# Optimization experiments

Hardware: AMD Instinct MI355X
Metric: run time of the kernel (lower is better)

Reference implementation:

```python
import jax, jax.numpy as jnp
import numpy as np

WS = (2, 7, 7)   # window size (d, h, w)
NH = 4           # num heads
EPS = 1e-5       # LayerNorm eps (torch default)


def _rel_index():
    wd, wh, ww = WS
    coords = np.stack(np.meshgrid(np.arange(wd), np.arange(wh), np.arange(ww), indexing='ij'))  # (3,wd,wh,ww)
    cf = coords.reshape(3, -1)                      # (3, N)
    rel = cf[:, :, None] - cf[:, None, :]           # (3, N, N)
    rel = rel.transpose(1, 2, 0).astype(np.int64)   # (N, N, 3)
    rel[..., 0] += wd - 1
    rel[..., 1] += wh - 1
    rel[..., 2] += ww - 1
    rel[..., 0] *= (2 * wh - 1) * (2 * ww - 1)
    rel[..., 1] *= (2 * ww - 1)
    return jnp.asarray(rel.sum(-1), dtype=jnp.int32)  # (N, N)


def setup_inputs() -> dict:
    key = jax.random.key(0)
    ks = jax.random.split(key, 6)
    C, CH = 128, 512
    TBL = (2 * WS[0] - 1) * (2 * WS[1] - 1) * (2 * WS[2] - 1)  # 507
    rn = lambda k, s, sc=0.02: jax.random.normal(k, s, jnp.float32) * sc
    return {
        'x': jax.random.normal(ks[0], (2, 8, 56, 56, C), jnp.float32),
        'norm1_w': jnp.ones((C,), jnp.float32), 'norm1_b': jnp.zeros((C,), jnp.float32),
        'qkv_w': rn(ks[1], (3 * C, C)), 'qkv_b': jnp.zeros((3 * C,), jnp.float32),
        'bias_table': rn(ks[2], (TBL, NH)),
        'proj_w': rn(ks[3], (C, C)), 'proj_b': jnp.zeros((C,), jnp.float32),
        'norm2_w': jnp.ones((C,), jnp.float32), 'norm2_b': jnp.zeros((C,), jnp.float32),
        'fc1_w': rn(ks[4], (CH, C)), 'fc1_b': jnp.zeros((CH,), jnp.float32),
        'fc2_w': rn(ks[5], (C, CH)), 'fc2_b': jnp.zeros((C,), jnp.float32),
        'rel_index': _rel_index(),
    }


def _layernorm(x, w, b):
    m = jnp.mean(x, axis=-1, keepdims=True)
    v = jnp.mean(jnp.square(x - m), axis=-1, keepdims=True)
    return (x - m) * jax.lax.rsqrt(v + EPS) * w + b


def reference(x, norm1_w, norm1_b, qkv_w, qkv_b, bias_table, proj_w, proj_b,
              norm2_w, norm2_b, fc1_w, fc1_b, fc2_w, fc2_b, rel_index):
    B, D, H, W, C = x.shape
    wd, wh, ww = WS
    N = wd * wh * ww
    hd = C // NH

    shortcut = x
    xn = _layernorm(x, norm1_w, norm1_b)
    # window partition: (B,D,H,W,C) -> (B*nW, N, C)
    xw = xn.reshape(B, D // wd, wd, H // wh, wh, W // ww, ww, C)
    xw = xw.transpose(0, 1, 3, 5, 2, 4, 6, 7).reshape(-1, N, C)
    B_ = xw.shape[0]

    qkv = (xw @ qkv_w.T + qkv_b).reshape(B_, N, 3, NH, hd).transpose(2, 0, 3, 1, 4)
    q, k, v = qkv[0] * (hd ** -0.5), qkv[1], qkv[2]   # (B_, NH, N, hd)
    attn = jnp.einsum('bhnd,bhmd->bhnm', q, k)
    bias = bias_table[rel_index.reshape(-1)].reshape(N, N, NH).transpose(2, 0, 1)  # (NH,N,N)
    attn = jax.nn.softmax(attn + bias[None], axis=-1)
    out = jnp.einsum('bhnm,bhmd->bhnd', attn, v).transpose(0, 2, 1, 3).reshape(B_, N, C)
    out = out @ proj_w.T + proj_b

    # window reverse: (B*nW, N, C) -> (B,D,H,W,C)
    xr = out.reshape(B, D // wd, H // wh, W // ww, wd, wh, ww, C)
    xr = xr.transpose(0, 1, 4, 2, 5, 3, 6, 7).reshape(B, D, H, W, C)

    x = shortcut + xr
    h = _layernorm(x, norm2_w, norm2_b)
    h = jax.nn.gelu(h @ fc1_w.T + fc1_b, approximate=False)  # torch nn.GELU = exact erf
    return x + (h @ fc2_w.T + fc2_b)
```

## Files before the change

### kernel.cpp

```cpp
#include <hip/hip_runtime.h>
#include <hip/hip_bf16.h>

typedef __hip_bfloat16 bf16;
typedef unsigned short u16t;
typedef unsigned int u32t;
typedef __attribute__((ext_vector_type(8))) short bf16x8_t;
typedef __attribute__((ext_vector_type(4))) float f32x4_t;

#define DEVI static __device__ __forceinline__

DEVI float u2f(u32t bits) { union { u32t u; float f; } v; v.u = bits; return v.f; }
DEVI float bflo(u32t u) { return u2f((u & 0xffffu) << 16); }
DEVI float bfhi(u32t u) { return u2f(u & 0xffff0000u); }
DEVI float sh2f(short s) { return u2f(((u32t)(u16t)s) << 16); }
DEVI float bf2f(bf16 h) { return __bfloat162float(h); }
DEVI bf16 f2bf(float f) { return __float2bfloat16(f); }
DEVI u16t f2bfbits(float f) {
  bf16 h = __float2bfloat16(f);
  union { bf16 h; u16t u; } v; v.h = h; return v.u;
}

DEVI void gl_lds16(const void* g, void* l) {
  __builtin_amdgcn_global_load_lds(
      (const __attribute__((address_space(1))) unsigned int*)g,
      (__attribute__((address_space(3))) unsigned int*)l, 16, 0, 0);
}

#define TOK   50176
#define NWIN  512
#define NTOK  98
#define NHEAD 4
#define HDIM  32
#define QSCALE 0.17677669529663687f

__global__ __launch_bounds__(256) void cvt4_k(
    const float* __restrict__ a, const float* __restrict__ b,
    const float* __restrict__ c, const float* __restrict__ d,
    bf16* __restrict__ o) {
  int i = blockIdx.x * 256 + threadIdx.x;
  const float* s; int off;
  if (i < 49152)       { s = a; off = 0; }
  else if (i < 65536)  { s = b; off = 49152; }
  else if (i < 131072) { s = c; off = 65536; }
  else                 { s = d; off = 131072; }
  float v = s[i - off];
  if (i < 16384) v *= QSCALE;
  o[i] = f2bf(v);
}

__global__ __launch_bounds__(256) void bias_k(const float* __restrict__ btab,
                                              const int* __restrict__ relidx,
                                              const float* __restrict__ qkv_b,
                                              float* __restrict__ BmatT,
                                              float* __restrict__ bsc) {
  int idx = blockIdx.x * 256 + threadIdx.x;
  if (idx < NTOK * NTOK) {
    int i = idx / NTOK, j = idx - i * NTOK;
    int r = relidx[idx] * NHEAD;
#pragma unroll
    for (int h = 0; h < NHEAD; h++)
      BmatT[(size_t)(h * NTOK + j) * 112 + i] = btab[r + h];
  }
  if (blockIdx.x == 0 && threadIdx.x < 384)
    bsc[threadIdx.x] = qkv_b[threadIdx.x] * (threadIdx.x < 128 ? QSCALE : 1.0f);
}

__global__ __launch_bounds__(256) void ln1_k(
    const float* __restrict__ x, const float* __restrict__ w,
    const float* __restrict__ b, bf16* __restrict__ o)
{
  const int wave = threadIdx.x >> 6, lane = threadIdx.x & 63;
  const int t = blockIdx.x * 4 + wave;
  const int c = lane << 1;
  float2 xv = *(const float2*)(x + (size_t)t * 128 + c);
  float x0 = xv.x, x1 = xv.y;
  float s = x0 + x1, ss = x0 * x0 + x1 * x1;
#pragma unroll
  for (int m = 32; m; m >>= 1) { s += __shfl_xor(s, m); ss += __shfl_xor(ss, m); }
  float mean = s * 0.0078125f;
  float var = ss * 0.0078125f - mean * mean;
  float rstd = rsqrtf(var + 1e-5f);
  float y0 = (x0 - mean) * rstd * w[c]     + b[c];
  float y1 = (x1 - mean) * rstd * w[c + 1] + b[c + 1];
  int wi = t % 56; int r = t / 56;
  int hi_ = r % 56; r /= 56;
  int di = r & 7; int bi = r >> 3;
  int nw = ((bi * 4 + (di >> 1)) * 8 + hi_ / 7) * 8 + wi / 7;
  int n  = ((di & 1) * 7 + hi_ % 7) * 7 + wi % 7;
  u32t ov = ((u32t)f2bfbits(y1) << 16) | (u32t)f2bfbits(y0);
  *(u32t*)((u16t*)o + (size_t)(nw * NTOK + n) * 128 + c) = ov;
}

DEVI int winrev(int grow) {
  int nw = grow / NTOK, n = grow - nw * NTOK;
  int wq = nw & 7, hq = (nw >> 3) & 7, dq = (nw >> 6) & 3, bb = nw >> 8;
  int wr = n % 7; int q7 = n / 7; int hr = q7 % 7, dr = q7 / 7;
  return ((bb * 8 + dq * 2 + dr) * 56 + hq * 7 + hr) * 56 + wq * 7 + wr;
}

template <int MODE, int NT16, int KT>
__global__ __launch_bounds__(256) void gemm3_k(
    const bf16* __restrict__ A, const bf16* __restrict__ W,
    const float* __restrict__ bias, const float* __restrict__ resX,
    const bf16* __restrict__ resB2, bf16* __restrict__ outB,
    bf16* __restrict__ outB2, float* __restrict__ outF,
    const float* __restrict__ lnw, const float* __restrict__ lnb, int N)
{
  __shared__ __align__(16) short As[128 * 128];
  __shared__ __align__(16) short Bs[NT16 * 16 * 128];
  const int K = KT * 128;
  const int tid = threadIdx.x;
  const int rowBase = blockIdx.y << 7;
  const int colBase = blockIdx.x * (NT16 * 16);
  const int wv = tid >> 6, lane = tid & 63;
  const int q = lane >> 4, r16 = lane & 15;
  const int mB = wv << 5;

  f32x4_t acc[2][NT16];
#pragma unroll
  for (int i = 0; i < 2; i++)
#pragma unroll
    for (int j = 0; j < NT16; j++) acc[i][j] = (f32x4_t){0.f, 0.f, 0.f, 0.f};

#pragma unroll
  for (int kt = 0; kt < KT; kt++) {
    const int kc = kt << 7;
#pragma unroll
    for (int t = 0; t < 8; t++) {
      int f = tid + (t << 8);
      int row = f >> 4, cs = (f & 15) ^ (row & 15);
      gl_lds16((const u16t*)A + (size_t)(rowBase + row) * K + kc + (cs << 3),
               &As[f << 3]);
    }
#pragma unroll
    for (int t = 0; t < NT16; t++) {
      int f = tid + (t << 8);
      int row = f >> 4, cs = (f & 15) ^ (row & 15);
      gl_lds16((const u16t*)W + (size_t)(colBase + row) * K + kc + (cs << 3),
               &Bs[f << 3]);
    }
    __syncthreads();
#pragma unroll
    for (int ks = 0; ks < 4; ks++) {
      bf16x8_t af[2], bfr[NT16];
#pragma unroll
      for (int mt = 0; mt < 2; mt++) {
        int row = mB + (mt << 4) + r16;
        int slot = ((ks << 2) + q) ^ (row & 15);
        af[mt] = *(const bf16x8_t*)&As[(row << 7) + (slot << 3)];
      }
#pragma unroll
      for (int nt = 0; nt < NT16; nt++) {
        int row = (nt << 4) + r16;
        int slot = ((ks << 2) + q) ^ (row & 15);
        bfr[nt] = *(const bf16x8_t*)&Bs[(row << 7) + (slot << 3)];
      }
#pragma unroll
      for (int mt = 0; mt < 2; mt++)
#pragma unroll
        for (int nt = 0; nt < NT16; nt++)
          acc[mt][nt] = __builtin_amdgcn_mfma_f32_16x16x32_bf16(
              af[mt], bfr[nt], acc[mt][nt], 0, 0, 0);
    }
    __syncthreads();
  }

  float bv[NT16];
#pragma unroll
  for (int nt = 0; nt < NT16; nt++) bv[nt] = bias[colBase + (nt << 4) + r16];

  if (MODE == 3) {
    float* Cf = (float*)As;
#pragma unroll
    for (int mt = 0; mt < 2; mt++)
#pragma unroll
      for (int reg = 0; reg < 4; reg++) {
        int lrow = mB + (mt << 4) + (q << 2) + reg;
#pragma unroll
        for (int nt = 0; nt < NT16; nt++)
          Cf[(lrow << 6) + (nt << 4) + r16] = acc[mt][nt][reg] + bv[nt];
      }
    __syncthreads();
#pragma unroll
    for (int t = 0; t < 8; t++) {
      int f = tid + (t << 8);
      int row = f >> 4, c4 = (f & 15) << 2;
      size_t ob = (size_t)(rowBase + row) * N + colBase + c4;
      const u16t* rp = (const u16t*)resB2 + ob;
      float4 v;
      v.x = Cf[(row << 6) + c4]     + sh2f(rp[0]);
      v.y = Cf[(row << 6) + c4 + 1] + sh2f(rp[1]);
      v.z = Cf[(row << 6) + c4 + 2] + sh2f(rp[2]);
      v.w = Cf[(row << 6) + c4 + 3] + sh2f(rp[3]);
      *(float4*)(outF + ob) = v;
    }
    return;
  }

  if (MODE == 1) {
#pragma unroll
    for (int mt = 0; mt < 2; mt++)
#pragma unroll
      for (int reg = 0; reg < 4; reg++) {
        int lrow = mB + (mt << 4) + (q << 2) + reg;
#pragma unroll
        for (int nt = 0; nt < NT16; nt++)
          As[(lrow << 7) + (nt << 4) + r16] = (short)f2bfbits(acc[mt][nt][reg] + bv[nt]);
      }
    __syncthreads();
#pragma unroll
    for (int t = 0; t < 8; t++) {
      int f = tid + (t << 8);
      int row = f >> 4, c8 = (f & 15) << 3;
      int tt = winrev(rowBase + row);
      size_t ob = (size_t)tt * 128 + c8;
      float4 r0 = *(const float4*)(resX + ob);
      float4 r1 = *(const float4*)(resX + ob + 4);
      short* cs = &As[(row << 7) + c8];
      u16t pk[8];
      pk[0] = f2bfbits(sh2f(cs[0]) + r0.x); pk[1] = f2bfbits(sh2f(cs[1]) + r0.y);
      pk[2] = f2bfbits(sh2f(cs[2]) + r0.z); pk[3] = f2bfbits(sh2f(cs[3]) + r0.w);
      pk[4] = f2bfbits(sh2f(cs[4]) + r1.x); pk[5] = f2bfbits(sh2f(cs[5]) + r1.y);
      pk[6] = f2bfbits(sh2f(cs[6]) + r1.z); pk[7] = f2bfbits(sh2f(cs[7]) + r1.w);
      *(uint4*)((u16t*)outB + ob) = *(const uint4*)pk;
      *(uint4*)cs = *(const uint4*)pk;
    }
    __syncthreads();
    const int c = lane << 1;
    float2 lw = *(const float2*)(lnw + c);
    float2 lb = *(const float2*)(lnb + c);
#pragma unroll 4
    for (int rr = 0; rr < 32; rr++) {
      int row = (wv << 5) + rr;
      u32t u = *(const u32t*)&As[(row << 7) + c];
      float x0 = bflo(u), x1 = bfhi(u);
      float s = x0 + x1, ss = x0 * x0 + x1 * x1;
#pragma unroll
      for (int m = 32; m; m >>= 1) { s += __shfl_xor(s, m); ss += __shfl_xor(ss, m); }
      float mean = s * 0.0078125f;
      float var = ss * 0.0078125f - mean * mean;
      float rstd = rsqrtf(var + 1e-5f);
      float y0 = (x0 - mean) * rstd * lw.x + lb.x;
      float y1 = (x1 - mean) * rstd * lw.y + lb.y;
      int tt = winrev(rowBase + row);
      u32t ov = ((u32t)f2bfbits(y1) << 16) | (u32t)f2bfbits(y0);
      *(u32t*)((u16t*)outB2 + (size_t)tt * 128 + c) = ov;
    }
    return;
  }

#pragma unroll
  for (int mt = 0; mt < 2; mt++)
#pragma unroll
    for (int reg = 0; reg < 4; reg++) {
      int lrow = mB + (mt << 4) + (q << 2) + reg;
#pragma unroll
      for (int nt = 0; nt < NT16; nt++) {
        float v = acc[mt][nt][reg] + bv[nt];
        if (MODE == 2) v = 0.5f * v * (1.0f + erff(v * 0.70710678118654752f));
        As[(lrow << 6) + (nt << 4) + r16] = (short)f2bfbits(v);
      }
    }
  __syncthreads();
#pragma unroll
  for (int t = 0; t < 4; t++) {
    int f = tid + (t << 8);
    int row = f >> 3, c8 = (f & 7) << 3;
    size_t ob = (size_t)(rowBase + row) * N + colBase + c8;
    *(uint4*)((u16t*)outB + ob) = *(const uint4*)&As[(row << 6) + c8];
  }
}

#define PSTR 136
__global__ __launch_bounds__(256) void attn_mfma_k(
    const bf16* __restrict__ qkv, const float* __restrict__ BmatT,
    bf16* __restrict__ out)
{
  __shared__ short Vt[32 * PSTR];
  __shared__ short Ps[112 * PSTR];
  const int nw = blockIdx.x, h = blockIdx.y;
  const int tid = threadIdx.x;
  const int wv = tid >> 6, lane = tid & 63;
  const int q = lane >> 4, r16 = lane & 15;

  for (int idx = tid; idx < 32 * 38; idx += 256) {
    int d = idx / 38, j = 98 + idx % 38;
    Vt[d * PSTR + j] = 0;
  }
  for (int idx = tid; idx < 112 * 12; idx += 256) {
    int r = idx / 12, c = (idx % 12) << 1;
    *(u32t*)&Ps[r * PSTR + 112 + c] = 0;
  }
  for (int idx = tid; idx < NTOK * 16; idx += 256) {
    int j = idx >> 4, d2 = (idx & 15) << 1;
    u32t uv = *(const u32t*)((const u16t*)qkv +
                             (size_t)(nw * NTOK + j) * 384 + 256 + h * 32 + d2);
    Vt[d2 * PSTR + j] = (short)(uv & 0xffffu);
    Vt[(d2 + 1) * PSTR + j] = (short)(uv >> 16);
  }
  __syncthreads();

  const int mt0 = wv;
  const bool has2 = (wv + 4) < 7;
  const int mt1 = has2 ? wv + 4 : wv;

  int i0 = mt0 * 16 + r16; if (i0 > NTOK - 1) i0 = NTOK - 1;
  int i1 = mt1 * 16 + r16; if (i1 > NTOK - 1) i1 = NTOK - 1;
  bf16x8_t aq0 = *(const bf16x8_t*)((const u16t*)qkv +
      (size_t)(nw * NTOK + i0) * 384 + h * 32 + (q << 3));
  bf16x8_t aq1 = *(const bf16x8_t*)((const u16t*)qkv +
      (size_t)(nw * NTOK + i1) * 384 + h * 32 + (q << 3));

  f32x4_t sc[2][7];
#pragma unroll
  for (int nt = 0; nt < 7; nt++) {
    int j = (nt << 4) + r16; if (j > NTOK - 1) j = NTOK - 1;
    const float* bRow = &BmatT[(size_t)(h * NTOK + j) * 112];
    bf16x8_t bk = *(const bf16x8_t*)((const u16t*)qkv +
        (size_t)(nw * NTOK + j) * 384 + 128 + h * 32 + (q << 3));
    f32x4_t b0 = *(const f32x4_t*)&bRow[mt0 * 16 + (q << 2)];
    f32x4_t b1 = *(const f32x4_t*)&bRow[mt1 * 16 + (q << 2)];
    sc[0][nt] = __builtin_amdgcn_mfma_f32_16x16x32_bf16(aq0, bk, b0, 0, 0, 0);
    sc[1][nt] = __builtin_amdgcn_mfma_f32_16x16x32_bf16(aq1, bk, b1, 0, 0, 0);
  }

#pragma unroll
  for (int sel = 0; sel < 2; sel++) {
    if (sel == 1 && !has2) break;
    int mtile = sel ? mt1 : mt0;
    int ibase = mtile * 16 + (q << 2);
    float s[4][7];
#pragma unroll
    for (int nt = 0; nt < 7; nt++) {
      int j = (nt << 4) + r16;
#pragma unroll
      for (int reg = 0; reg < 4; reg++) {
        int i = ibase + reg;
        s[reg][nt] = (i < NTOK && j < NTOK) ? sc[sel][nt][reg] : -1.0e30f;
      }
    }
#pragma unroll
    for (int reg = 0; reg < 4; reg++) {
      float m = -3.0e38f;
#pragma unroll
      for (int nt = 0; nt < 7; nt++) m = fmaxf(m, s[reg][nt]);
#pragma unroll
      for (int d = 8; d; d >>= 1) m = fmaxf(m, __shfl_xor(m, d));
      float sum = 0.f;
#pragma unroll
      for (int nt = 0; nt < 7; nt++) { s[reg][nt] = __expf(s[reg][nt] - m); sum += s[reg][nt]; }
#pragma unroll
      for (int d = 8; d; d >>= 1) sum += __shfl_xor(sum, d);
      float inv = 1.f / sum;
#pragma unroll
      for (int nt = 0; nt < 7; nt++)
        Ps[(ibase + reg) * PSTR + (nt << 4) + r16] =
            (short)f2bfbits(s[reg][nt] * inv);
    }
    f32x4_t o0 = {0.f, 0.f, 0.f, 0.f}, o1 = {0.f, 0.f, 0.f, 0.f};
#pragma unroll
    for (int kt = 0; kt < 4; kt++) {
      bf16x8_t ap = *(const bf16x8_t*)&Ps[(mtile * 16 + r16) * PSTR + (kt << 5) + (q << 3)];
      bf16x8_t bv0 = *(const bf16x8_t*)&Vt[r16 * PSTR + (kt << 5) + (q << 3)];
      bf16x8_t bv1 = *(const bf16x8_t*)&Vt[(16 + r16) * PSTR + (kt << 5) + (q << 3)];
      o0 = __builtin_amdgcn_mfma_f32_16x16x32_bf16(ap, bv0, o0, 0, 0, 0);
      o1 = __builtin_amdgcn_mfma_f32_16x16x32_bf16(ap, bv1, o1, 0, 0, 0);
    }
#pragma unroll
    for (int reg = 0; reg < 4; reg++) {
      int i = mtile * 16 + (q << 2) + reg;
      if (i < NTOK) {
        size_t ob = (size_t)(nw * NTOK + i) * 128 + h * 32;
        out[ob + r16] = f2bf(o0[reg]);
        out[ob + 16 + r16] = f2bf(o1[reg]);
      }
    }
  }
}

extern "C" void kernel_launch(void* const* d_in, const int* in_sizes, int n_in,
                              void* d_out, int out_size, void* d_ws, size_t ws_size,
                              hipStream_t stream) {
  const float* x      = (const float*)d_in[0];
  const float* n1w    = (const float*)d_in[1];
  const float* n1b    = (const float*)d_in[2];
  const float* qkv_w  = (const float*)d_in[3];
  const float* qkv_b  = (const float*)d_in[4];
  const float* btab   = (const float*)d_in[5];
  const float* proj_w = (const float*)d_in[6];
  const float* proj_b = (const float*)d_in[7];
  const float* n2w    = (const float*)d_in[8];
  const float* n2b    = (const float*)d_in[9];
  const float* fc1_w  = (const float*)d_in[10];
  const float* fc1_b  = (const float*)d_in[11];
  const float* fc2_w  = (const float*)d_in[12];
  const float* fc2_b  = (const float*)d_in[13];
  const int*   relidx = (const int*)d_in[14];

  const size_t Asz = (size_t)TOK * 128 * 2;
  char* ws = (char*)d_ws;
  bf16* wbf   = (bf16*)ws;
  bf16* qkvw16  = wbf;
  bf16* projw16 = wbf + 49152;
  bf16* fc1w16  = wbf + 65536;
  bf16* fc2w16  = wbf + 131072;
  float* BmatT = (float*)(ws + 393216);
  float* bsc   = (float*)(ws + 393216 + 175616);
  char* R = ws + (1 << 20);
  bf16* xw    = (bf16*)d_out;
  bf16* attn  = (bf16*)d_out;
  bf16* qkv   = (bf16*)R;
  bf16* x2    = (bf16*)R;
  bf16* xn2   = (bf16*)(R + Asz);
  bf16* hmid  = (bf16*)(R + 2 * Asz);
  float* out  = (float*)d_out;
  const bool fullM = ws_size >= ((size_t)(1 << 20) + 6 * Asz);

  cvt4_k<<<768, 256, 0, stream>>>(qkv_w, proj_w, fc1_w, fc2_w, wbf);
  bias_k<<<38, 256, 0, stream>>>(btab, relidx, qkv_b, BmatT, bsc);
  ln1_k<<<TOK / 4, 256, 0, stream>>>(x, n1w, n1b, xw);
  gemm3_k<0, 4, 1><<<dim3(6, TOK / 128), 256, 0, stream>>>(
      xw, qkvw16, bsc, nullptr, nullptr, qkv, nullptr, nullptr,
      nullptr, nullptr, 384);
  attn_mfma_k<<<dim3(NWIN, NHEAD), 256, 0, stream>>>(qkv, BmatT, attn);
  gemm3_k<1, 8, 1><<<dim3(1, TOK / 128), 256, 0, stream>>>(
      attn, projw16, proj_b, x, nullptr, x2, xn2, nullptr, n2w, n2b, 128);
  if (fullM) {
    gemm3_k<2, 4, 1><<<dim3(8, TOK / 128), 256, 0, stream>>>(
        xn2, fc1w16, fc1_b, nullptr, nullptr, hmid, nullptr, nullptr,
        nullptr, nullptr, 512);
    gemm3_k<3, 4, 4><<<dim3(2, TOK / 128), 256, 0, stream>>>(
        hmid, fc2w16, fc2_b, nullptr, x2, nullptr, nullptr, out,
        nullptr, nullptr, 128);
  } else {
    const int MC = TOK / 4;
    for (int c = 0; c < 4; c++) {
      gemm3_k<2, 4, 1><<<dim3(8, MC / 128), 256, 0, stream>>>(
          xn2 + (size_t)c * MC * 128, fc1w16, fc1_b, nullptr, nullptr,
          hmid, nullptr, nullptr, nullptr, nullptr, 512);
      gemm3_k<3, 4, 4><<<dim3(2, MC / 128), 256, 0, stream>>>(
          hmid, fc2w16, fc2_b, nullptr, x2 + (size_t)c * MC * 128,
          nullptr, nullptr, out + (size_t)c * MC * 128, nullptr, nullptr, 128);
    }
  }
}
```

Baseline: 234.9 us.

## Fuse fc1, GELU and fc2 into one MLP kernel keeping hidden in LDS

Replaces the separate fc1+GELU and fc2+residual GEMM launches with a single kernel. Each block holds a 128-row activation tile, streams 64-column chunks of fc1 and fc2 weights, computes the GELU hidden chunk into LDS and accumulates fc2 output in registers. This removes the round trip of the 512-wide hidden tensor through global memory and one launch. In exchange, weight loads are not double-buffered, the kernel needs 80KB of LDS per block, and the fc1 N-parallelism is lost, so occupancy and grid size (TOK/128 blocks) drop.

```diff
diff --git a/kernel.cpp b/kernel.cpp
--- a/kernel.cpp
+++ b/kernel.cpp
@@ -169,34 +169,6 @@
 #pragma unroll
   for (int nt = 0; nt < NT16; nt++) bv[nt] = bias[colBase + (nt << 4) + r16];
 
-  if (MODE == 3) {
-    float* Cf = (float*)As;
-#pragma unroll
-    for (int mt = 0; mt < 2; mt++)
-#pragma unroll
-      for (int reg = 0; reg < 4; reg++) {
-        int lrow = mB + (mt << 4) + (q << 2) + reg;
-#pragma unroll
-        for (int nt = 0; nt < NT16; nt++)
-          Cf[(lrow << 6) + (nt << 4) + r16] = acc[mt][nt][reg] + bv[nt];
-      }
-    __syncthreads();
-#pragma unroll
-    for (int t = 0; t < 8; t++) {
-      int f = tid + (t << 8);
-      int row = f >> 4, c4 = (f & 15) << 2;
-      size_t ob = (size_t)(rowBase + row) * N + colBase + c4;
-      const u16t* rp = (const u16t*)resB2 + ob;
-      float4 v;
-      v.x = Cf[(row << 6) + c4]     + sh2f(rp[0]);
-      v.y = Cf[(row << 6) + c4 + 1] + sh2f(rp[1]);
-      v.z = Cf[(row << 6) + c4 + 2] + sh2f(rp[2]);
-      v.w = Cf[(row << 6) + c4 + 3] + sh2f(rp[3]);
-      *(float4*)(outF + ob) = v;
-    }
-    return;
-  }
-
   if (MODE == 1) {
 #pragma unroll
     for (int mt = 0; mt < 2; mt++)
@@ -257,7 +229,6 @@
 #pragma unroll
       for (int nt = 0; nt < NT16; nt++) {
         float v = acc[mt][nt][reg] + bv[nt];
-        if (MODE == 2) v = 0.5f * v * (1.0f + erff(v * 0.70710678118654752f));
         As[(lrow << 6) + (nt << 4) + r16] = (short)f2bfbits(v);
       }
     }
@@ -268,6 +239,173 @@
     int row = f >> 3, c8 = (f & 7) << 3;
     size_t ob = (size_t)(rowBase + row) * N + colBase + c8;
     *(uint4*)((u16t*)outB + ob) = *(const uint4*)&As[(row << 6) + c8];
+  }
+}
+
+__global__ __launch_bounds__(256, 2) void mlp_fused_k(
+    const bf16* __restrict__ Axn, const bf16* __restrict__ F1,
+    const bf16* __restrict__ F2, const float* __restrict__ b1,
+    const float* __restrict__ b2, const bf16* __restrict__ resB,
+    float* __restrict__ out)
+{
+  __shared__ __align__(16) char smem[81920];
+  short* As  = (short*)smem;
+  short* F1s = (short*)(smem + 32768);
+  short* F2s = (short*)(smem + 49152);
+  short* Hs  = (short*)(smem + 65536);
+  float* Cf  = (float*)smem;
+
+  const int tid = threadIdx.x;
+  const int rowBase = blockIdx.x << 7;
+  const int wv = tid >> 6, lane = tid & 63;
+  const int q = lane >> 4, r16 = lane & 15;
+  const int mB = wv << 5;
+
+#pragma unroll
+  for (int t = 0; t < 8; t++) {
+    int f = tid + (t << 8);
+    int row = f >> 4, cs = (f & 15) ^ (row & 15);
+    gl_lds16((const u16t*)Axn + (size_t)(rowBase + row) * 128 + (cs << 3),
+             &As[f << 3]);
+  }
+#pragma unroll
+  for (int t = 0; t < 4; t++) {
+    int f = tid + (t << 8);
+    int row = f >> 4, cs = (f & 15) ^ (row & 15);
+    gl_lds16((const u16t*)F1 + (size_t)row * 128 + (cs << 3), &F1s[f << 3]);
+  }
+#pragma unroll
+  for (int t = 0; t < 4; t++) {
+    int f = tid + (t << 8);
+    int row = f >> 3, cs = (f & 7) ^ (row & 7);
+    gl_lds16((const u16t*)F2 + (size_t)row * 512 + (cs << 3), &F2s[f << 3]);
+  }
+  __syncthreads();
+
+  f32x4_t oacc[2][8];
+#pragma unroll
+  for (int i = 0; i < 2; i++)
+#pragma unroll
+    for (int j = 0; j < 8; j++) oacc[i][j] = (f32x4_t){0.f, 0.f, 0.f, 0.f};
+
+#pragma unroll 1
+  for (int c = 0; c < 8; c++) {
+    if (c > 0) {
+#pragma unroll
+      for (int t = 0; t < 4; t++) {
+        int f = tid + (t << 8);
+        int row = f >> 4, cs = (f & 15) ^ (row & 15);
+        gl_lds16((const u16t*)F1 + (size_t)(c * 64 + row) * 128 + (cs << 3),
+                 &F1s[f << 3]);
+      }
+#pragma unroll
+      for (int t = 0; t < 4; t++) {
+        int f = tid + (t << 8);
+        int row = f >> 3, cs = (f & 7) ^ (row & 7);
+        gl_lds16((const u16t*)F2 + (size_t)row * 512 + c * 64 + (cs << 3),
+                 &F2s[f << 3]);
+      }
+      __syncthreads();
+    }
+
+    f32x4_t hacc[2][4];
+#pragma unroll
+    for (int i = 0; i < 2; i++)
+#pragma unroll
+      for (int j = 0; j < 4; j++) hacc[i][j] = (f32x4_t){0.f, 0.f, 0.f, 0.f};
+#pragma unroll
+    for (int ks = 0; ks < 4; ks++) {
+      bf16x8_t af[2], bfr[4];
+#pragma unroll
+      for (int mt = 0; mt < 2; mt++) {
+        int row = mB + (mt << 4) + r16;
+        int slot = ((ks << 2) + q) ^ (row & 15);
+        af[mt] = *(const bf16x8_t*)&As[(row << 7) + (slot << 3)];
+      }
+#pragma unroll
+      for (int nt = 0; nt < 4; nt++) {
+        int row = (nt << 4) + r16;
+        int slot = ((ks << 2) + q) ^ (row & 15);
+        bfr[nt] = *(const bf16x8_t*)&F1s[(row << 7) + (slot << 3)];
+      }
+#pragma unroll
+      for (int mt = 0; mt < 2; mt++)
+#pragma unroll
+        for (int nt = 0; nt < 4; nt++)
+          hacc[mt][nt] = __builtin_amdgcn_mfma_f32_16x16x32_bf16(
+              af[mt], bfr[nt], hacc[mt][nt], 0, 0, 0);
+    }
+
+    float bb[4];
+#pragma unroll
+    for (int nt = 0; nt < 4; nt++) bb[nt] = b1[c * 64 + (nt << 4) + r16];
+#pragma unroll
+    for (int mt = 0; mt < 2; mt++)
+#pragma unroll
+      for (int reg = 0; reg < 4; reg++) {
+        int lrow = mB + (mt << 4) + (q << 2) + reg;
+#pragma unroll
+        for (int nt = 0; nt < 4; nt++) {
+          float v = hacc[mt][nt][reg] + bb[nt];
+          v = 0.5f * v * (1.0f + erff(v * 0.70710678118654752f));
+          int col = (nt << 4) + r16;
+          int sp = (col >> 3) ^ (lrow & 7);
+          Hs[(lrow << 6) + (sp << 3) + (col & 7)] = (short)f2bfbits(v);
+        }
+      }
+    __syncthreads();
+
+#pragma unroll
+    for (int ks = 0; ks < 2; ks++) {
+      bf16x8_t af[2], bfr[8];
+#pragma unroll
+      for (int mt = 0; mt < 2; mt++) {
+        int row = mB + (mt << 4) + r16;
+        int slot = ((ks << 2) + q) ^ (row & 7);
+        af[mt] = *(const bf16x8_t*)&Hs[(row << 6) + (slot << 3)];
+      }
+#pragma unroll
+      for (int nt = 0; nt < 8; nt++) {
+        int row = (nt << 4) + r16;
+        int slot = ((ks << 2) + q) ^ (row & 7);
+        bfr[nt] = *(const bf16x8_t*)&F2s[(row << 6) + (slot << 3)];
+      }
+#pragma unroll
+      for (int mt = 0; mt < 2; mt++)
+#pragma unroll
+        for (int nt = 0; nt < 8; nt++)
+          oacc[mt][nt] = __builtin_amdgcn_mfma_f32_16x16x32_bf16(
+              af[mt], bfr[nt], oacc[mt][nt], 0, 0, 0);
+    }
+    __syncthreads();
+  }
+
+  float bv[8];
+#pragma unroll
+  for (int nt = 0; nt < 8; nt++) bv[nt] = b2[(nt << 4) + r16];
+#pragma unroll
+  for (int mt = 0; mt < 2; mt++)
+#pragma unroll
+    for (int reg = 0; reg < 4; reg++) {
+      int lrow = mB + (mt << 4) + (q << 2) + reg;
+#pragma unroll
+      for (int nt = 0; nt < 8; nt++)
+        Cf[lrow * 132 + (nt << 4) + r16] = oacc[mt][nt][reg] + bv[nt];
+    }
+  __syncthreads();
+#pragma unroll
+  for (int t = 0; t < 16; t++) {
+    int f = tid + (t << 8);
+    int row = f >> 5, c4 = (f & 31) << 2;
+    size_t ob = (size_t)(rowBase + row) * 128 + c4;
+    const u16t* rp = (const u16t*)resB + ob;
+    const float* cp = &Cf[row * 132 + c4];
+    float4 v;
+    v.x = cp[0] + sh2f(rp[0]);
+    v.y = cp[1] + sh2f(rp[1]);
+    v.z = cp[2] + sh2f(rp[2]);
+    v.w = cp[3] + sh2f(rp[3]);
+    *(float4*)(out + ob) = v;
   }
 }
 
@@ -412,9 +550,7 @@
   bf16* qkv   = (bf16*)R;
   bf16* x2    = (bf16*)R;
   bf16* xn2   = (bf16*)(R + Asz);
-  bf16* hmid  = (bf16*)(R + 2 * Asz);
   float* out  = (float*)d_out;
-  const bool fullM = ws_size >= ((size_t)(1 << 20) + 6 * Asz);
 
   cvt4_k<<<768, 256, 0, stream>>>(qkv_w, proj_w, fc1_w, fc2_w, wbf);
   bias_k<<<38, 256, 0, stream>>>(btab, relidx, qkv_b, BmatT, bsc);
@@ -425,22 +561,6 @@
   attn_mfma_k<<<dim3(NWIN, NHEAD), 256, 0, stream>>>(qkv, BmatT, attn);
   gemm3_k<1, 8, 1><<<dim3(1, TOK / 128), 256, 0, stream>>>(
       attn, projw16, proj_b, x, nullptr, x2, xn2, nullptr, n2w, n2b, 128);
-  if (fullM) {
-    gemm3_k<2, 4, 1><<<dim3(8, TOK / 128), 256, 0, stream>>>(
-        xn2, fc1w16, fc1_b, nullptr, nullptr, hmid, nullptr, nullptr,
-        nullptr, nullptr, 512);
-    gemm3_k<3, 4, 4><<<dim3(2, TOK / 128), 256, 0, stream>>>(
-        hmid, fc2w16, fc2_b, nullptr, x2, nullptr, nullptr, out,
-        nullptr, nullptr, 128);
-  } else {
-    const int MC = TOK / 4;
-    for (int c = 0; c < 4; c++) {
-      gemm3_k<2, 4, 1><<<dim3(8, MC / 128), 256, 0, stream>>>(
-          xn2 + (size_t)c * MC * 128, fc1w16, fc1_b, nullptr, nullptr,
-          hmid, nullptr, nullptr, nullptr, nullptr, 512);
-      gemm3_k<3, 4, 4><<<dim3(2, MC / 128), 256, 0, stream>>>(
-          hmid, fc2w16, fc2_b, nullptr, x2 + (size_t)c * MC * 128,
-          nullptr, nullptr, out + (size_t)c * MC * 128, nullptr, nullptr, 128);
-    }
-  }
-}
+  mlp_fused_k<<<TOK / 128, 256, 0, stream>>>(
+      xn2, fc1w16, fc2w16, fc1_b, fc2_b, x2, out);
+}
```

After: 218.3 us. 7.1% less time.
